# Kernel tuning notes

Hardware: AMD Instinct MI355X
Metric: run time of the kernel (lower is better)

The kernel has to match this reference:

```python
import jax, jax.numpy as jnp
import numpy as np

N, D, L = 524288, 64, 20  # tokens, in_features, chain depth (20 Linear layers per branch)


def setup_inputs() -> dict:
    key = jax.random.key(0)
    kx, kw, kb = jax.random.split(key, 3)
    x = jax.random.normal(kx, (N, D), dtype=jnp.float32)
    # torch.nn.Linear default init: U(-1/sqrt(fan_in), 1/sqrt(fan_in))
    bound = 1.0 / np.sqrt(D)
    W = jax.random.uniform(kw, (L, D, D), dtype=jnp.float32, minval=-bound, maxval=bound)
    b = jax.random.uniform(kb, (L, D), dtype=jnp.float32, minval=-bound, maxval=bound)
    return {"x": x, "W": W, "b": b}


def reference(x, W, b):
    # is_hit=False => scatter routes ALL tokens to path 1 (path 0 is empty),
    # so forward = branches[1]: 20 sequential Linear(D, D) layers, then a
    # trivial gather (concat of the single non-empty branch result).
    # torch Linear: y = x @ W^T + b, W has shape [out, in].
    def step(h, wb):
        w, bias = wb  # w: [D, D], bias: [D]
        return h @ w.T + bias, None

    out, _ = jax.lax.scan(step, x, (W, b))
    return out
```

## Files before the change

### kernel.cpp

```cpp
#include <hip/hip_runtime.h>
#include <stdint.h>


using short8  = __attribute__((ext_vector_type(8))) short;
using floatx4 = __attribute__((ext_vector_type(4))) float;

#define N_TOK   524288
#define N_LAYER 20

__device__ __forceinline__ uint32_t pk_bf16(float lo, float hi) {
  uint32_t a = __float_as_uint(lo) + 0x8000u;
  uint32_t b = __float_as_uint(hi) + 0x8000u;
  return (b & 0xffff0000u) | (a >> 16);
}

__device__ __forceinline__ uint16_t bf16_rne(float f) {
  uint32_t u = __float_as_uint(f);
  u += 0x7fffu + ((u >> 16) & 1u);
  return (uint16_t)(u >> 16);
}

__global__ void prep_weights(const float* __restrict__ W, uint16_t* __restrict__ ws) {
  int idx  = blockIdx.x * 256 + threadIdx.x;
  int l    = idx >> 9;
  int rem  = idx & 511;
  int frag = rem >> 6;
  int lane = rem & 63;
  int mt = frag >> 1, ks = frag & 1;
  int m  = lane & 15;
  int q  = lane >> 4;
  int wrow = 32 * (mt >> 1) + 8 * (m >> 2) + 4 * (mt & 1) + (m & 3);
  int k0   = 32 * ks + 8 * q;
  const float* src = W + l * 4096 + wrow * 64 + k0;
  float4 f0 = *(const float4*)(src);
  float4 f1 = *(const float4*)(src + 4);
  union { uint16_t s[8]; uint4 v; } o;
  o.s[0] = bf16_rne(f0.x); o.s[1] = bf16_rne(f0.y);
  o.s[2] = bf16_rne(f0.z); o.s[3] = bf16_rne(f0.w);
  o.s[4] = bf16_rne(f1.x); o.s[5] = bf16_rne(f1.y);
  o.s[6] = bf16_rne(f1.z); o.s[7] = bf16_rne(f1.w);
  *(uint4*)(ws + (size_t)idx * 8) = o.v;
}

union BFrag { short8 v; uint32_t u[4]; };

__global__ __launch_bounds__(256, 2) void chain_fused(
    const float* __restrict__ x, const uint16_t* __restrict__ wf,
    const float* __restrict__ bias, float* __restrict__ out)
{
  __shared__ uint4 wbuf[2][512];
  __shared__ __align__(16) float biasLds[N_LAYER * 64];

  const int tid  = threadIdx.x;
  const int wv   = tid >> 6;
  const int lane = tid & 63;
  const int tl   = lane & 15;
  const int q    = lane >> 4;
  const int tokbase = blockIdx.x * 256 + wv * 64;

  for (int i = tid; i < N_LAYER * 64; i += 256) biasLds[i] = bias[i];

  {
    const uint4* s = (const uint4*)wf + tid * 2;
    wbuf[0][tid * 2]     = s[0];
    wbuf[0][tid * 2 + 1] = s[1];
  }

  BFrag Bf[4][2];
  #pragma unroll
  for (int tb = 0; tb < 4; tb++) {
    const float* xp = x + (size_t)(tokbase + tb * 16 + tl) * 64 + 8 * q;
    #pragma unroll
    for (int ks = 0; ks < 2; ks++) {
      float4 a0 = *(const float4*)(xp + 32 * ks);
      float4 a1 = *(const float4*)(xp + 32 * ks + 4);
      Bf[tb][ks].u[0] = pk_bf16(a0.x, a0.y);
      Bf[tb][ks].u[1] = pk_bf16(a0.z, a0.w);
      Bf[tb][ks].u[2] = pk_bf16(a1.x, a1.y);
      Bf[tb][ks].u[3] = pk_bf16(a1.z, a1.w);
    }
  }
  __syncthreads();

  floatx4 acc[4][4];
  int cur = 0;
  #pragma unroll 2
  for (int l = 0; l < N_LAYER; l++) {
    uint4 pv0, pv1;
    if (l + 1 < N_LAYER) {
      const uint4* s = (const uint4*)wf + (size_t)(l + 1) * 512 + tid * 2;
      pv0 = s[0]; pv1 = s[1];
    }

    short8 Af[8];
    const short8* ap = (const short8*)&wbuf[cur][0];
    #pragma unroll
    for (int f = 0; f < 8; f++) Af[f] = ap[f * 64 + lane];

    #pragma unroll
    for (int mt = 0; mt < 4; mt++) {
      floatx4 bv = *(const floatx4*)(biasLds + l * 64 + 32 * (mt >> 1) + 4 * (mt & 1) + 8 * q);
      #pragma unroll
      for (int tb = 0; tb < 4; tb++) acc[tb][mt] = bv;
    }

    #pragma unroll
    for (int ks = 0; ks < 2; ks++)
      #pragma unroll
      for (int mt = 0; mt < 4; mt++)
        #pragma unroll
        for (int tb = 0; tb < 4; tb++)
          acc[tb][mt] = __builtin_amdgcn_mfma_f32_16x16x32_bf16(
              Af[mt * 2 + ks], Bf[tb][ks].v, acc[tb][mt], 0, 0, 0);

    if (l == N_LAYER - 1) break;

    #pragma unroll
    for (int tb = 0; tb < 4; tb++)
      #pragma unroll
      for (int mt = 0; mt < 4; mt++) {
        const int ksn = mt >> 1;
        const int d   = 2 * (mt & 1);
        Bf[tb][ksn].u[d]     = pk_bf16(acc[tb][mt][0], acc[tb][mt][1]);
        Bf[tb][ksn].u[d + 1] = pk_bf16(acc[tb][mt][2], acc[tb][mt][3]);
      }

    wbuf[cur ^ 1][tid * 2]     = pv0;
    wbuf[cur ^ 1][tid * 2 + 1] = pv1;
    __syncthreads();
    cur ^= 1;
  }

  #pragma unroll
  for (int tb = 0; tb < 4; tb++) {
    float* op = out + (size_t)(tokbase + tb * 16 + tl) * 64;
    #pragma unroll
    for (int mt = 0; mt < 4; mt++)
      *(floatx4*)(op + 32 * (mt >> 1) + 4 * (mt & 1) + 8 * q) = acc[tb][mt];
  }
}

extern "C" void kernel_launch(void* const* d_in, const int* in_sizes, int n_in,
                              void* d_out, int out_size, void* d_ws, size_t ws_size,
                              hipStream_t stream) {
  (void)in_sizes; (void)n_in; (void)out_size; (void)ws_size;
  const float* x = (const float*)d_in[0];
  const float* W = (const float*)d_in[1];
  const float* b = (const float*)d_in[2];
  float* out = (float*)d_out;
  uint16_t* ws = (uint16_t*)d_ws;

  prep_weights<<<dim3(40), dim3(256), 0, stream>>>(W, ws);
  chain_fused<<<dim3(N_TOK / 256), dim3(256), 0, stream>>>(x, ws, b, out);
}
```

Baseline: 276.8 us.

## Load weight fragments directly from global into registers, drop LDS double buffer and barriers

Each wave now loads the next layer's weight fragments straight from global memory (L2/L1-cached) into registers, replacing the shared-memory double buffer and its per-layer __syncthreads. The bf16 packing uses the hardware cvt_pk_bf16 builtin when the compiler offers it, and a byte-permute otherwise. The occupancy hint is raised from 2 to 3 blocks per CU. This removes barrier stalls and LDS traffic but adds 8 uint4 prefetch registers per thread and more global load traffic per wave, which may cause register pressure at the higher occupancy target.

```diff
diff --git a/kernel.cpp b/kernel.cpp
--- a/kernel.cpp
+++ b/kernel.cpp
@@ -8,11 +8,26 @@
 #define N_TOK   524288
 #define N_LAYER 20
 
+#ifdef __has_builtin
+#if __has_builtin(__builtin_amdgcn_cvt_pk_bf16_f32)
+#define HAVE_CVT_PK_BF16 1
+#endif
+#endif
+
+#ifdef HAVE_CVT_PK_BF16
+typedef __bf16 bf16x2_t __attribute__((ext_vector_type(2)));
+__device__ __forceinline__ uint32_t pk_bf16(float lo, float hi) {
+  union { bf16x2_t v; uint32_t u; } c;
+  c.v = __builtin_amdgcn_cvt_pk_bf16_f32(lo, hi);
+  return c.u;
+}
+#else
 __device__ __forceinline__ uint32_t pk_bf16(float lo, float hi) {
   uint32_t a = __float_as_uint(lo) + 0x8000u;
   uint32_t b = __float_as_uint(hi) + 0x8000u;
-  return (b & 0xffff0000u) | (a >> 16);
+  return __builtin_amdgcn_perm(b, a, 0x07060302u);
 }
+#endif
 
 __device__ __forceinline__ uint16_t bf16_rne(float f) {
   uint32_t u = __float_as_uint(f);
@@ -43,12 +58,12 @@
 }
 
 union BFrag { short8 v; uint32_t u[4]; };
+union AFrag { short8 v; uint4 raw; };
 
-__global__ __launch_bounds__(256, 2) void chain_fused(
+__global__ __launch_bounds__(256, 3) void chain_fused(
     const float* __restrict__ x, const uint16_t* __restrict__ wf,
     const float* __restrict__ bias, float* __restrict__ out)
 {
-  __shared__ uint4 wbuf[2][512];
   __shared__ __align__(16) float biasLds[N_LAYER * 64];
 
   const int tid  = threadIdx.x;
@@ -59,12 +74,6 @@
   const int tokbase = blockIdx.x * 256 + wv * 64;
 
   for (int i = tid; i < N_LAYER * 64; i += 256) biasLds[i] = bias[i];
-
-  {
-    const uint4* s = (const uint4*)wf + tid * 2;
-    wbuf[0][tid * 2]     = s[0];
-    wbuf[0][tid * 2 + 1] = s[1];
-  }
 
   BFrag Bf[4][2];
   #pragma unroll
@@ -80,22 +89,21 @@
       Bf[tb][ks].u[3] = pk_bf16(a1.z, a1.w);
     }
   }
+
+  const uint4* wp = (const uint4*)wf;
+  AFrag Af[8];
+  #pragma unroll
+  for (int f = 0; f < 8; f++) Af[f].raw = wp[f * 64 + lane];
+
   __syncthreads();
 
   floatx4 acc[4][4];
-  int cur = 0;
   #pragma unroll 2
   for (int l = 0; l < N_LAYER; l++) {
-    uint4 pv0, pv1;
-    if (l + 1 < N_LAYER) {
-      const uint4* s = (const uint4*)wf + (size_t)(l + 1) * 512 + tid * 2;
-      pv0 = s[0]; pv1 = s[1];
-    }
-
-    short8 Af[8];
-    const short8* ap = (const short8*)&wbuf[cur][0];
+    const int ln = (l + 1 < N_LAYER) ? l + 1 : N_LAYER - 1;
+    uint4 nf[8];
     #pragma unroll
-    for (int f = 0; f < 8; f++) Af[f] = ap[f * 64 + lane];
+    for (int f = 0; f < 8; f++) nf[f] = wp[(ln * 8 + f) * 64 + lane];
 
     #pragma unroll
     for (int mt = 0; mt < 4; mt++) {
@@ -111,7 +119,7 @@
         #pragma unroll
         for (int tb = 0; tb < 4; tb++)
           acc[tb][mt] = __builtin_amdgcn_mfma_f32_16x16x32_bf16(
-              Af[mt * 2 + ks], Bf[tb][ks].v, acc[tb][mt], 0, 0, 0);
+              Af[mt * 2 + ks].v, Bf[tb][ks].v, acc[tb][mt], 0, 0, 0);
 
     if (l == N_LAYER - 1) break;
 
@@ -125,10 +133,8 @@
         Bf[tb][ksn].u[d + 1] = pk_bf16(acc[tb][mt][2], acc[tb][mt][3]);
       }
 
-    wbuf[cur ^ 1][tid * 2]     = pv0;
-    wbuf[cur ^ 1][tid * 2 + 1] = pv1;
-    __syncthreads();
-    cur ^= 1;
+    #pragma unroll
+    for (int f = 0; f < 8; f++) Af[f].raw = nf[f];
   }
 
   #pragma unroll
```

Result: no change. 277.8 us (+0.4%).
